# Optimization experiments

Hardware: AMD Instinct MI355X
Metric: run time of the kernel (lower is better)

Reference implementation:

```python
import jax, jax.numpy as jnp
import numpy as np

B, L, D, W = 4, 256, 256, 8  # batch, seq_len, d_model, context_window
NS_EPS = 1e-7


def setup_inputs() -> dict:
    key = jax.random.key(0)
    ks = jax.random.split(key, 12)
    f = lambda k, s: jax.random.normal(k, s, dtype=jnp.float32)
    sD = 1.0 / np.sqrt(D)
    return {
        "x": f(ks[0], (B, L, D)),
        "k_aligned": jnp.tanh(f(ks[1], (B, L, D))),  # QKProjectionLayer applies tanh upstream
        "v": f(ks[2], (B, L, D)),
        "M_prev": f(ks[3], (B, D, D)) * 0.01,
        "S_prev": jnp.zeros((B, D, D), jnp.float32),
        # polynomial feature coeffs: phi(k) = c1*k + c2*k^2 (degree 2, dim-preserving)
        "poly_coeffs": jnp.stack([jnp.ones((D,), jnp.float32), 0.1 * jnp.ones((D,), jnp.float32)])
        + 0.01 * f(ks[4], (2, D)),
        "alpha_W": f(ks[5], (D, D)) * sD, "alpha_b": jnp.zeros((D,), jnp.float32),
        "eta_W": f(ks[6], (D, D)) * sD, "eta_b": jnp.zeros((D,), jnp.float32),
        "theta_W": f(ks[7], (D, D)) * sD, "theta_b": jnp.zeros((D,), jnp.float32),
        "gamma_W": f(ks[8], (D,)) * sD, "gamma_b": jnp.zeros((1,), jnp.float32),
        "out_W": f(ks[9], (D, D)) * sD, "out_b": jnp.zeros((D,), jnp.float32),
    }


def _newton_schulz_1(S):
    # NS_K with K=1: X <- 1.5*X - 0.5*X X^T X after Frobenius normalization
    norm = jnp.sqrt(jnp.sum(S * S, axis=(-2, -1), keepdims=True)) + NS_EPS
    X = S / norm
    return 1.5 * X - 0.5 * jnp.einsum('bij,bkj,bkl->bil', X, X, X)


def reference(x, k_aligned, v, M_prev, S_prev, poly_coeffs,
              alpha_W, alpha_b, eta_W, eta_b, theta_W, theta_b,
              gamma_W, gamma_b, out_W, out_b):
    Bn, Ln, Dn = x.shape
    # polynomial feature layer (dim-preserving, degree 2)
    k_phi = poly_coeffs[0] * k_aligned + poly_coeffs[1] * k_aligned ** 2  # [B,L,D]
    # per-token gates (precomputed, pure linear+sigmoid)
    alpha = jax.nn.sigmoid(x @ alpha_W.T + alpha_b)          # [B,L,D]
    eta = jax.nn.sigmoid(x @ eta_W.T + eta_b) * 0.1          # [B,L,D]
    theta = jax.nn.sigmoid(x @ theta_W.T + theta_b)          # [B,L,D]
    gamma = jax.nn.sigmoid(jnp.einsum('bld,d->bl', x, gamma_W) + gamma_b[0])  # [B,L]
    c_arr = jnp.minimum(jnp.arange(Ln) + 1, W).astype(x.dtype)  # actual window length per step

    to_t = lambda a: jnp.moveaxis(a, 1, 0)  # [B,L,...] -> [L,B,...]
    xs = (to_t(k_phi), to_t(v), to_t(gamma), to_t(alpha), to_t(eta), to_t(theta), c_arr)

    buf_k = jnp.zeros((Bn, W, Dn), x.dtype)  # sliding window of phi(k); zero pads contribute 0
    buf_v = jnp.zeros((Bn, W, Dn), x.dtype)
    buf_g = jnp.zeros((Bn, W), x.dtype)

    def step(carry, xt):
        M, S, bk, bv, bg = carry
        k_t, v_t, g_t, a_t, e_t, th_t, c_t = xt
        bk = jnp.concatenate([bk[:, 1:], k_t[:, None]], axis=1)
        bv = jnp.concatenate([bv[:, 1:], v_t[:, None]], axis=1)
        bg = jnp.concatenate([bg[:, 1:], g_t[:, None]], axis=1)
        # Omega gradient: sum_i gamma_i * (M phi(k_i) - v_i) outer phi(k_i) / c
        pred = jnp.einsum('bde,bwe->bwd', M, bk)
        err = pred - bv
        grad = jnp.einsum('bw,bwd,bwe->bde', bg, err, bk) / c_t
        S = th_t[..., None] * S + grad
        S_ortho = _newton_schulz_1(S)
        M = a_t[..., None] * M - e_t[..., None] * S_ortho
        y = jnp.einsum('bde,be->bd', M, k_t)
        return (M, S, bk, bv, bg), y

    (M, S, _, _, _), ys = jax.lax.scan(step, (M_prev, S_prev, buf_k, buf_v, buf_g), xs)
    output = jnp.moveaxis(ys, 0, 1) @ out_W.T + out_b  # out_proj per token
    return (output, M, S)
```

## Files before the change

### kernel.cpp

```cpp
#include <hip/hip_runtime.h>

#define Bn 4
#define Ln 256
#define Dn 256
#define Wn 8
#define NBLK 64
#define BLD (Bn*Ln*Dn)
#define BDD (Bn*Dn*Dn)

typedef float  floatx4 __attribute__((ext_vector_type(4)));
typedef short  short8  __attribute__((ext_vector_type(8)));

__device__ __forceinline__ float ldc(const float* p) {
    return __hip_atomic_load(p, __ATOMIC_RELAXED, __HIP_MEMORY_SCOPE_AGENT);
}
__device__ __forceinline__ void stc(float* p, float v) {
    __hip_atomic_store(p, v, __ATOMIC_RELAXED, __HIP_MEMORY_SCOPE_AGENT);
}
__device__ __forceinline__ void stc4(float* p, floatx4 v) {
    asm volatile("global_store_dwordx4 %0, %1, off sc0 sc1" :: "v"(p), "v"(v) : "memory");
}
__device__ __forceinline__ void ldc4x4(floatx4& a0, floatx4& a1, floatx4& a2, floatx4& a3,
    const float* p0, const float* p1, const float* p2, const float* p3)
{
    asm volatile(
        "global_load_dwordx4 %0, %4, off sc0 sc1\n\t"
        "global_load_dwordx4 %1, %5, off sc0 sc1\n\t"
        "global_load_dwordx4 %2, %6, off sc0 sc1\n\t"
        "global_load_dwordx4 %3, %7, off sc0 sc1\n\t"
        "s_waitcnt vmcnt(0)"
        : "=&v"(a0), "=&v"(a1), "=&v"(a2), "=&v"(a3)
        : "v"(p0), "v"(p1), "v"(p2), "v"(p3)
        : "memory");
}
__device__ __forceinline__ void ldc4x8(
    floatx4& a0, floatx4& a1, floatx4& a2, floatx4& a3,
    floatx4& b0, floatx4& b1, floatx4& b2, floatx4& b3,
    const float* p0, const float* p1, const float* p2, const float* p3,
    const float* q0, const float* q1, const float* q2, const float* q3)
{
    asm volatile(
        "global_load_dwordx4 %0, %8, off sc0 sc1\n\t"
        "global_load_dwordx4 %1, %9, off sc0 sc1\n\t"
        "global_load_dwordx4 %2, %10, off sc0 sc1\n\t"
        "global_load_dwordx4 %3, %11, off sc0 sc1\n\t"
        "global_load_dwordx4 %4, %12, off sc0 sc1\n\t"
        "global_load_dwordx4 %5, %13, off sc0 sc1\n\t"
        "global_load_dwordx4 %6, %14, off sc0 sc1\n\t"
        "global_load_dwordx4 %7, %15, off sc0 sc1\n\t"
        "s_waitcnt vmcnt(0)"
        : "=&v"(a0), "=&v"(a1), "=&v"(a2), "=&v"(a3),
          "=&v"(b0), "=&v"(b1), "=&v"(b2), "=&v"(b3)
        : "v"(p0), "v"(p1), "v"(p2), "v"(p3),
          "v"(q0), "v"(q1), "v"(q2), "v"(q3)
        : "memory");
}
__device__ __forceinline__ void ldc1x8(
    float& d0, float& d1, float& d2, float& d3,
    float& d4, float& d5, float& d6, float& d7,
    const float* p0, const float* p1, const float* p2, const float* p3,
    const float* p4, const float* p5, const float* p6, const float* p7)
{
    asm volatile(
        "global_load_dword %0, %8, off sc0 sc1\n\t"
        "global_load_dword %1, %9, off sc0 sc1\n\t"
        "global_load_dword %2, %10, off sc0 sc1\n\t"
        "global_load_dword %3, %11, off sc0 sc1\n\t"
        "global_load_dword %4, %12, off sc0 sc1\n\t"
        "global_load_dword %5, %13, off sc0 sc1\n\t"
        "global_load_dword %6, %14, off sc0 sc1\n\t"
        "global_load_dword %7, %15, off sc0 sc1\n\t"
        "s_waitcnt vmcnt(0)"
        : "=&v"(d0), "=&v"(d1), "=&v"(d2), "=&v"(d3),
          "=&v"(d4), "=&v"(d5), "=&v"(d6), "=&v"(d7)
        : "v"(p0), "v"(p1), "v"(p2), "v"(p3),
          "v"(p4), "v"(p5), "v"(p6), "v"(p7)
        : "memory");
}

__device__ __forceinline__ unsigned f2bf(float x) {
    unsigned u = __float_as_uint(x);
    return (u + 0x7FFFu + ((u >> 16) & 1u)) >> 16;
}
__device__ __forceinline__ unsigned long long packbf4(floatx4 v) {
    unsigned lo = f2bf(v[0]) | (f2bf(v[1]) << 16);
    unsigned hi = f2bf(v[2]) | (f2bf(v[3]) << 16);
    return (unsigned long long)lo | ((unsigned long long)hi << 32);
}

__device__ __forceinline__ void grid_sync(unsigned* flags, unsigned k)
{
    asm volatile("s_waitcnt vmcnt(0) lgkmcnt(0)" ::: "memory");
    __syncthreads();
    if (threadIdx.x == 0)
        __hip_atomic_store(&flags[(unsigned)blockIdx.x * 32u], k,
                           __ATOMIC_RELAXED, __HIP_MEMORY_SCOPE_AGENT);
    if (threadIdx.x < NBLK) {
        while (__hip_atomic_load(&flags[(unsigned)threadIdx.x * 32u],
                                 __ATOMIC_RELAXED, __HIP_MEMORY_SCOPE_AGENT) < k)
            __builtin_amdgcn_s_sleep(1);
    }
    __syncthreads();
}

__global__ __launch_bounds__(256) void kphi_gamma_kernel(
    const float* __restrict__ k_al, const float* __restrict__ x,
    const float* __restrict__ poly, const float* __restrict__ gW,
    const float* __restrict__ gb, float* __restrict__ kphi,
    float* __restrict__ gamma)
{
    int wg = blockIdx.x, tid = threadIdx.x;
    int wave = tid >> 6, lane = tid & 63;
    int n = wg * 4 + wave;
    float gacc = 0.f;
#pragma unroll
    for (int c = 0; c < 4; ++c) {
        int e = lane + 64 * c;
        float kv = k_al[n * Dn + e];
        kphi[n * Dn + e] = poly[e] * kv + poly[Dn + e] * kv * kv;
        gacc += x[n * Dn + e] * gW[e];
    }
#pragma unroll
    for (int off = 32; off; off >>= 1) gacc += __shfl_xor(gacc, off);
    if (lane == 0) gamma[n] = 1.f / (1.f + expf(-(gacc + gb[0])));
}

template <int ACT>
__global__ __launch_bounds__(256) void gemm_act_kernel(
    const float* __restrict__ In, const float* __restrict__ Wm,
    const float* __restrict__ bias, float* __restrict__ Out)
{
    __shared__ float ldsX[32 * 64];
    __shared__ float ldsW[64 * 65];
    int n0 = blockIdx.x * 32;
    int m0 = blockIdx.y * 64;
    int tid = threadIdx.x;
    float acc[8] = {0, 0, 0, 0, 0, 0, 0, 0};
    for (int j0 = 0; j0 < 256; j0 += 64) {
#pragma unroll
        for (int q = 0; q < 2; ++q) {
            int fi = tid + 256 * q; int row = fi >> 4; int c4 = (fi & 15) << 2;
            *(float4*)&ldsX[row * 64 + c4] =
                *(const float4*)&In[(n0 + row) * 256 + j0 + c4];
        }
#pragma unroll
        for (int q = 0; q < 4; ++q) {
            int fi = tid + 256 * q; int row = fi >> 4; int c4 = (fi & 15) << 2;
            float4 vv = *(const float4*)&Wm[(m0 + row) * 256 + j0 + c4];
            ldsW[(c4 + 0) * 65 + row] = vv.x;
            ldsW[(c4 + 1) * 65 + row] = vv.y;
            ldsW[(c4 + 2) * 65 + row] = vv.z;
            ldsW[(c4 + 3) * 65 + row] = vv.w;
        }
        __syncthreads();
        int m = tid & 63, ng = tid >> 6;
        for (int j = 0; j < 64; ++j) {
            float wv = ldsW[j * 65 + m];
#pragma unroll
            for (int r = 0; r < 8; ++r) acc[r] += ldsX[(ng * 8 + r) * 64 + j] * wv;
        }
        __syncthreads();
    }
    int m = tid & 63, ng = tid >> 6;
    float bv = bias[m0 + m];
#pragma unroll
    for (int r = 0; r < 8; ++r) {
        float vv = acc[r] + bv;
        if (ACT == 1) vv = 1.f / (1.f + expf(-vv));
        if (ACT == 2) vv = 0.1f / (1.f + expf(-vv));
        Out[(n0 + ng * 8 + r) * 256 + m0 + m] = vv;
    }
}

__global__ __launch_bounds__(256) void prologue_kernel(
    const float* __restrict__ Mprev, const float* __restrict__ Sprev,
    float* __restrict__ M, float* __restrict__ S, float* __restrict__ ST,
    float* __restrict__ ys, float* __restrict__ normbuf,
    unsigned* __restrict__ flags)
{
    int gidx = blockIdx.x * 256 + threadIdx.x;
    ((float4*)M)[gidx] = ((const float4*)Mprev)[gidx];
    ((float4*)S)[gidx] = ((const float4*)Sprev)[gidx];
    float4 z = {0.f, 0.f, 0.f, 0.f};
    ((float4*)ys)[gidx] = z;
    {
        int o = gidx * 4;
        int bb = o >> 16, rm = o & 65535, l = rm >> 8, k = rm & 255;
        float4 stv;
        stv.x = Sprev[bb * 65536 + (k + 0) * 256 + l];
        stv.y = Sprev[bb * 65536 + (k + 1) * 256 + l];
        stv.z = Sprev[bb * 65536 + (k + 2) * 256 + l];
        stv.w = Sprev[bb * 65536 + (k + 3) * 256 + l];
        ((float4*)ST)[gidx] = stv;
    }
    if (gidx < Ln * Bn) normbuf[gidx] = 0.f;
    if (gidx < NBLK * 32) flags[gidx] = 0u;
}

__global__ void __launch_bounds__(256, 1) scan_kernel(
    const float* __restrict__ kphi, const float* __restrict__ vin,
    const float* __restrict__ gammaB, const float* __restrict__ alphaB,
    const float* __restrict__ etaB, const float* __restrict__ thetaB,
    float* __restrict__ Mg, float* __restrict__ Sg, float* __restrict__ STg,
    float* __restrict__ T0g, float* __restrict__ T1g,
    float* __restrict__ u_buf, float* __restrict__ a_buf,
    float* __restrict__ K_buf, float* __restrict__ normbuf,
    float* __restrict__ ysg, unsigned* __restrict__ flags)
{
    __shared__ float smem[11072];
    const int wg = blockIdx.x, tid = threadIdx.x;
    const int b = wg >> 4;
    const int rem = wg & 15;
    const int i0 = (rem >> 2) * 64, l0 = (rem & 3) * 64;
    const int d0 = rem << 4;
    const int wid = tid >> 6, lane = tid & 63;
    const int rb = (tid >> 4) << 2;
    const int kb = (tid & 15) << 2;
    char* TtB  = (char*)(smem + 6464);
    char* StlB = (char*)(smem + 8768);
    unsigned kbar = 0;

    {
        floatx4 acc[4];
#pragma unroll
        for (int lt = 0; lt < 4; ++lt) acc[lt] = (floatx4){0.f, 0.f, 0.f, 0.f};
        const float* Sb = Sg + (size_t)b * Dn * Dn;
        for (int kc = 0; kc < 256; kc += 64) {
            floatx4 t0, t1, t2, t3, s0, s1, s2, s3;
            ldc4x8(t0, t1, t2, t3, s0, s1, s2, s3,
                   &Sb[(i0 + rb + 0) * Dn + kc + kb], &Sb[(i0 + rb + 1) * Dn + kc + kb],
                   &Sb[(i0 + rb + 2) * Dn + kc + kb], &Sb[(i0 + rb + 3) * Dn + kc + kb],
                   &Sb[(l0 + rb + 0) * Dn + kc + kb], &Sb[(l0 + rb + 1) * Dn + kc + kb],
                   &Sb[(l0 + rb + 2) * Dn + kc + kb], &Sb[(l0 + rb + 3) * Dn + kc + kb]);
            *(unsigned long long*)(TtB + (rb + 0) * 144 + kb * 2) = packbf4(t0);
            *(unsigned long long*)(TtB + (rb + 1) * 144 + kb * 2) = packbf4(t1);
            *(unsigned long long*)(TtB + (rb + 2) * 144 + kb * 2) = packbf4(t2);
            *(unsigned long long*)(TtB + (rb + 3) * 144 + kb * 2) = packbf4(t3);
            *(unsigned long long*)(StlB + (rb + 0) * 144 + kb * 2) = packbf4(s0);
            *(unsigned long long*)(StlB + (rb + 1) * 144 + kb * 2) = packbf4(s1);
            *(unsigned long long*)(StlB + (rb + 2) * 144 + kb * 2) = packbf4(s2);
            *(unsigned long long*)(StlB + (rb + 3) * 144 + kb * 2) = packbf4(s3);
            __syncthreads();
            const int arow = wid * 16 + (lane & 15);
#pragma unroll
            for (int ks = 0; ks < 2; ++ks) {
                const int kloc = ks * 32 + ((lane >> 4) << 3);
                short8 af = *(const short8*)(TtB + arow * 144 + kloc * 2);
#pragma unroll
                for (int lt = 0; lt < 4; ++lt) {
                    short8 bf = *(const short8*)(StlB + (lt * 16 + (lane & 15)) * 144 + kloc * 2);
                    acc[lt] = __builtin_amdgcn_mfma_f32_16x16x32_bf16(af, bf, acc[lt], 0, 0, 0);
                }
            }
            __syncthreads();
        }
        const int ibr = i0 + wid * 16 + ((lane >> 4) << 2);
        const int lc = lane & 15;
#pragma unroll
        for (int lt = 0; lt < 4; ++lt)
#pragma unroll
            for (int g = 0; g < 4; ++g)
                stc(&T0g[((size_t)b * Dn + ibr + g) * Dn + l0 + lt * 16 + lc], acc[lt][g]);
    }
    grid_sync(flags, ++kbar);

    for (int t = 0; t < Ln; ++t) {
        const int cwin = (t + 1 < Wn) ? (t + 1) : Wn;
        const float invc = 1.f / (float)cwin;

        {
            float* kW  = smem;
            float* Mst = smem + 2080;
            float* Sst = smem + 6240;
            float* us  = smem + 10400;
            float* as_ = smem + 10528;
            float* ths = smem + 10656;
#pragma unroll
            for (int q = 0; q < 2; ++q) {
                int w = q * 4 + (tid >> 6);
                int c4 = (tid & 63) << 2;
                int tk = t - 7 + w;
                floatx4 kv = {0.f, 0.f, 0.f, 0.f};
                if (tk >= 0) kv = *(const floatx4*)&kphi[(b * Ln + tk) * Dn + c4];
                *(floatx4*)&kW[w * 260 + c4] = kv;
            }
            if (tid < 16) ths[tid] = thetaB[(b * Ln + t) * Dn + d0 + tid];
            {
                const float* mb = &Mg[((size_t)b * Dn + d0) * Dn];
                const float* sb = &Sg[((size_t)b * Dn + d0) * Dn];
                int ra = tid >> 6, c4 = (tid & 63) << 2;
                floatx4 m0, m1, m2, m3, s0, s1, s2, s3;
                ldc4x8(m0, m1, m2, m3, s0, s1, s2, s3,
                       &mb[(ra + 0) * Dn + c4], &mb[(ra + 4) * Dn + c4],
                       &mb[(ra + 8) * Dn + c4], &mb[(ra + 12) * Dn + c4],
                       &sb[(ra + 0) * Dn + c4], &sb[(ra + 4) * Dn + c4],
                       &sb[(ra + 8) * Dn + c4], &sb[(ra + 12) * Dn + c4]);
                *(floatx4*)&Mst[(ra + 0) * 260 + c4] = m0;
                *(floatx4*)&Mst[(ra + 4) * 260 + c4] = m1;
                *(floatx4*)&Mst[(ra + 8) * 260 + c4] = m2;
                *(floatx4*)&Mst[(ra + 12) * 260 + c4] = m3;
                *(floatx4*)&Sst[(ra + 0) * 260 + c4] = s0;
                *(floatx4*)&Sst[(ra + 4) * 260 + c4] = s1;
                *(floatx4*)&Sst[(ra + 8) * 260 + c4] = s2;
                *(floatx4*)&Sst[(ra + 12) * 260 + c4] = s3;
            }
            __syncthreads();
            {
                const int w = tid >> 5, r = (tid >> 1) & 15, eh = tid & 1;
                const int eb = eh * 128;
                float em = 0.f, eq = 0.f;
                for (int j = 0; j < 128; j += 4) {
                    floatx4 kv = *(const floatx4*)&kW[w * 260 + eb + j];
                    floatx4 mv = *(const floatx4*)&Mst[r * 260 + eb + j];
                    floatx4 sv = *(const floatx4*)&Sst[r * 260 + eb + j];
                    em += kv[0] * mv[0] + kv[1] * mv[1] + kv[2] * mv[2] + kv[3] * mv[3];
                    eq += kv[0] * sv[0] + kv[1] * sv[1] + kv[2] * sv[2] + kv[3] * sv[3];
                }
                em += __shfl_xor(em, 1);
                eq += __shfl_xor(eq, 1);
                if (eh == 0) {
                    int tok = t - 7 + w;
                    float uu = 0.f;
                    if (tok >= 0) {
                        float ev = em - vin[(b * Ln + tok) * Dn + d0 + r];
                        uu = gammaB[b * Ln + tok] * invc * ev;
                    }
                    float aa = ths[r] * eq;
                    us[w * 16 + r] = uu;
                    as_[w * 16 + r] = aa;
                    stc(&u_buf[(b * 8 + w) * Dn + d0 + r], uu);
                    stc(&a_buf[(b * 8 + w) * Dn + d0 + r], aa);
                }
            }
            if (rem == 0 && tid < 64) {
                int wa = tid >> 3, wb2 = tid & 7;
                float g = 0.f;
                for (int j = 0; j < 256; j += 4) {
                    floatx4 x1 = *(const floatx4*)&kW[wa * 260 + j];
                    floatx4 x2 = *(const floatx4*)&kW[wb2 * 260 + j];
                    g += x1[0] * x2[0] + x1[1] * x2[1] + x1[2] * x2[2] + x1[3] * x2[3];
                }
                stc(&K_buf[b * 64 + tid], g);
            }
            __syncthreads();
            float* Snew = Mst;
            {
                int r = tid >> 4, m = tid & 15;
                float th = ths[r];
                float uu[8];
#pragma unroll
                for (int w = 0; w < 8; ++w) uu[w] = us[w * 16 + r];
                float sumsq = 0.f;
                for (int c = 0; c < 16; ++c) {
                    int e = m + 16 * c;
                    float sv = th * Sst[r * 260 + e];
#pragma unroll
                    for (int w = 0; w < 8; ++w) sv += uu[w] * kW[w * 260 + e];
                    Snew[r * 260 + e] = sv;
                    sumsq += sv * sv;
                }
#pragma unroll
                for (int off = 32; off; off >>= 1) sumsq += __shfl_xor(sumsq, off);
                if ((tid & 63) == 0) atomicAdd(&normbuf[t * Bn + b], sumsq);
            }
            __syncthreads();
            {
                int r = tid >> 4, ec = (tid & 15) * 16;
                float* Sp = &Sg[((size_t)b * Dn + d0 + r) * Dn + ec];
#pragma unroll
                for (int c = 0; c < 4; ++c)
                    stc4(&Sp[c * 4], *(floatx4*)&Snew[r * 260 + ec + c * 4]);
            }
            {
                int lq = tid >> 4, r = tid & 15;
#pragma unroll
                for (int j = 0; j < 16; ++j) {
                    int l = lq * 16 + j;
                    stc(&STg[((size_t)b * Dn + l) * Dn + d0 + r], Snew[r * 260 + l]);
                }
            }
        }
        grid_sync(flags, ++kbar);

        {
            float* uv  = smem;
            float* av  = smem + 2048;
            float* cv  = smem + 4096;
            float* thv = smem + 6144;
            float* Kl  = smem + 6400;
            const float* Told = ((t & 1) ? T1g : T0g) + (size_t)b * Dn * Dn;
            float*       Tnew = ((t & 1) ? T0g : T1g) + (size_t)b * Dn * Dn;
            const float* STb = STg + (size_t)b * Dn * Dn;
            float nrmsq = ldc(&normbuf[t * Bn + b]);
            {
                int fi0 = tid, fi1 = 256 + tid, fi2 = tid, fi3 = 256 + tid;
                floatx4 v0, v1, v2, v3;
                ldc4x4(v0, v1, v2, v3,
                       &u_buf[b * 2048 + fi0 * 4], &u_buf[b * 2048 + fi1 * 4],
                       &a_buf[b * 2048 + fi2 * 4], &a_buf[b * 2048 + fi3 * 4]);
                *(floatx4*)&uv[fi0 * 4] = v0;
                *(floatx4*)&uv[fi1 * 4] = v1;
                *(floatx4*)&av[fi2 * 4] = v2;
                *(floatx4*)&av[fi3 * 4] = v3;
                if (tid < 64) {
                    *(floatx4*)&thv[tid * 4] = *(const floatx4*)&thetaB[(b * Ln + t) * Dn + tid * 4];
                    Kl[tid] = ldc(&K_buf[b * 64 + tid]);
                }
            }
            __syncthreads();
#pragma unroll
            for (int q = 0; q < 8; ++q) {
                int idx = q * 256 + tid;
                int w = idx >> 8, e = idx & 255;
                float s = av[idx];
#pragma unroll
                for (int w2 = 0; w2 < 8; ++w2) s += 0.5f * Kl[w * 8 + w2] * uv[w2 * 256 + e];
                cv[idx] = s;
            }
            __syncthreads();
            floatx4 acc[4];
#pragma unroll
            for (int lt = 0; lt < 4; ++lt) acc[lt] = (floatx4){0.f, 0.f, 0.f, 0.f};
            for (int kc = 0; kc < 256; kc += 64) {
                floatx4 tv0, tv1, tv2, tv3, s0, s1, s2, s3;
                ldc4x8(tv0, tv1, tv2, tv3, s0, s1, s2, s3,
                       &Told[(i0 + rb + 0) * Dn + kc + kb], &Told[(i0 + rb + 1) * Dn + kc + kb],
                       &Told[(i0 + rb + 2) * Dn + kc + kb], &Told[(i0 + rb + 3) * Dn + kc + kb],
                       &STb[(l0 + rb + 0) * Dn + kc + kb], &STb[(l0 + rb + 1) * Dn + kc + kb],
                       &STb[(l0 + rb + 2) * Dn + kc + kb], &STb[(l0 + rb + 3) * Dn + kc + kb]);
                floatx4 tvv[4] = {tv0, tv1, tv2, tv3};
                floatx4 thk = *(floatx4*)&thv[kc + kb];
#pragma unroll
                for (int x = 0; x < 4; ++x) {
                    float thi = thv[i0 + rb + x];
                    tvv[x] = (thi * thk) * tvv[x];
                }
#pragma unroll
                for (int w = 0; w < 8; ++w) {
                    floatx4 ui = *(floatx4*)&uv[w * 256 + i0 + rb];
                    floatx4 ci = *(floatx4*)&cv[w * 256 + i0 + rb];
                    floatx4 uk = *(floatx4*)&uv[w * 256 + kc + kb];
                    floatx4 ck = *(floatx4*)&cv[w * 256 + kc + kb];
#pragma unroll
                    for (int x = 0; x < 4; ++x)
                        tvv[x] += ui[x] * ck + ci[x] * uk;
                }
                if (l0 == 0) {
#pragma unroll
                    for (int x = 0; x < 4; ++x)
                        stc4(&Tnew[(i0 + rb + x) * Dn + kc + kb], tvv[x]);
                }
                floatx4 svv_[4] = {s0, s1, s2, s3};
#pragma unroll
                for (int x = 0; x < 4; ++x) {
                    *(unsigned long long*)(TtB + (rb + x) * 144 + kb * 2) = packbf4(tvv[x]);
                    *(unsigned long long*)(StlB + (rb + x) * 144 + kb * 2) = packbf4(svv_[x]);
                }
                __syncthreads();
                const int arow = wid * 16 + (lane & 15);
#pragma unroll
                for (int ks = 0; ks < 2; ++ks) {
                    const int kloc = ks * 32 + ((lane >> 4) << 3);
                    short8 af = *(const short8*)(TtB + arow * 144 + kloc * 2);
#pragma unroll
                    for (int lt = 0; lt < 4; ++lt) {
                        short8 bf = *(const short8*)(StlB + (lt * 16 + (lane & 15)) * 144 + kloc * 2);
                        acc[lt] = __builtin_amdgcn_mfma_f32_16x16x32_bf16(af, bf, acc[lt], 0, 0, 0);
                    }
                }
                __syncthreads();
            }
            {
                float nrm = sqrtf(nrmsq) + 1e-7f;
                float inv_n = 1.f / nrm;
                float w1 = 1.5f * inv_n;
                float w3 = 0.5f * inv_n * inv_n * inv_n;
                const int ibr = i0 + wid * 16 + ((lane >> 4) << 2);
                const int lc = lane & 15;
                float* Mb = Mg + (size_t)b * Dn * Dn;
                const float* sp[16]; float* mp[16];
#pragma unroll
                for (int lt = 0; lt < 4; ++lt)
#pragma unroll
                    for (int g = 0; g < 4; ++g) {
                        int l = l0 + lt * 16 + lc;
                        sp[lt * 4 + g] = &STb[l * Dn + ibr + g];
                        mp[lt * 4 + g] = &Mb[(ibr + g) * Dn + l];
                    }
                float svv[16], mvv[16];
                ldc1x8(svv[0], svv[1], svv[2], svv[3], svv[4], svv[5], svv[6], svv[7],
                       sp[0], sp[1], sp[2], sp[3], sp[4], sp[5], sp[6], sp[7]);
                ldc1x8(svv[8], svv[9], svv[10], svv[11], svv[12], svv[13], svv[14], svv[15],
                       sp[8], sp[9], sp[10], sp[11], sp[12], sp[13], sp[14], sp[15]);
                ldc1x8(mvv[0], mvv[1], mvv[2], mvv[3], mvv[4], mvv[5], mvv[6], mvv[7],
                       mp[0], mp[1], mp[2], mp[3], mp[4], mp[5], mp[6], mp[7]);
                ldc1x8(mvv[8], mvv[9], mvv[10], mvv[11], mvv[12], mvv[13], mvv[14], mvv[15],
                       mp[8], mp[9], mp[10], mp[11], mp[12], mp[13], mp[14], mp[15]);
                float alv[4], etv[4];
#pragma unroll
                for (int g = 0; g < 4; ++g) {
                    alv[g] = alphaB[(b * Ln + t) * Dn + ibr + g];
                    etv[g] = etaB[(b * Ln + t) * Dn + ibr + g];
                }
                float kvr[4];
#pragma unroll
                for (int lt = 0; lt < 4; ++lt)
                    kvr[lt] = kphi[(b * Ln + t) * Dn + l0 + lt * 16 + lc];
                float py[4] = {0.f, 0.f, 0.f, 0.f};
#pragma unroll
                for (int lt = 0; lt < 4; ++lt)
#pragma unroll
                    for (int g = 0; g < 4; ++g) {
                        int idx = lt * 4 + g;
                        float ns = w1 * svv[idx] - w3 * acc[lt][g];
                        float mn = alv[g] * mvv[idx] - etv[g] * ns;
                        stc(mp[idx], mn);
                        py[g] += mn * kvr[lt];
                    }
#pragma unroll
                for (int g = 0; g < 4; ++g) {
                    float p = py[g];
                    p += __shfl_xor(p, 1); p += __shfl_xor(p, 2);
                    p += __shfl_xor(p, 4); p += __shfl_xor(p, 8);
                    if (lc == 0) atomicAdd(&ysg[(b * Ln + t) * Dn + ibr + g], p);
                }
            }
        }
        grid_sync(flags, ++kbar);
    }
}

extern "C" void kernel_launch(void* const* d_in, const int* in_sizes, int n_in,
                              void* d_out, int out_size, void* d_ws, size_t ws_size,
                              hipStream_t stream)
{
    const float* x       = (const float*)d_in[0];
    const float* k_al    = (const float*)d_in[1];
    const float* v       = (const float*)d_in[2];
    const float* M_prev  = (const float*)d_in[3];
    const float* S_prev  = (const float*)d_in[4];
    const float* poly    = (const float*)d_in[5];
    const float* alpha_W = (const float*)d_in[6];
    const float* alpha_b = (const float*)d_in[7];
    const float* eta_W   = (const float*)d_in[8];
    const float* eta_b   = (const float*)d_in[9];
    const float* theta_W = (const float*)d_in[10];
    const float* theta_b = (const float*)d_in[11];
    const float* gamma_W = (const float*)d_in[12];
    const float* gamma_b = (const float*)d_in[13];
    const float* out_W   = (const float*)d_in[14];
    const float* out_b   = (const float*)d_in[15];

    float* ws = (float*)d_ws;
    float* kphi    = ws;
    float* alphaB  = kphi   + BLD;
    float* etaB    = alphaB + BLD;
    float* thetaB  = etaB   + BLD;
    float* gammaB  = thetaB + BLD;
    float* STws    = gammaB + Bn * Ln;
    float* T0ws    = STws   + BDD;
    float* T1ws    = T0ws   + BDD;
    float* ysws    = T1ws   + BDD;
    float* u_bufp  = ysws   + BLD;
    float* a_bufp  = u_bufp + Bn*Wn*Dn;
    float* K_bufp  = a_bufp + Bn*Wn*Dn;
    float* normbuf = K_bufp + Bn*64;
    unsigned* flags = (unsigned*)(normbuf + Ln * Bn);

    float* out_y = (float*)d_out;
    float* Mout  = out_y + BLD;
    float* Sout  = Mout + BDD;

    hipLaunchKernelGGL(kphi_gamma_kernel, dim3(256), dim3(256), 0, stream,
                       k_al, x, poly, gamma_W, gamma_b, kphi, gammaB);
    hipLaunchKernelGGL((gemm_act_kernel<1>), dim3(32, 4), dim3(256), 0, stream,
                       x, alpha_W, alpha_b, alphaB);
    hipLaunchKernelGGL((gemm_act_kernel<2>), dim3(32, 4), dim3(256), 0, stream,
                       x, eta_W, eta_b, etaB);
    hipLaunchKernelGGL((gemm_act_kernel<1>), dim3(32, 4), dim3(256), 0, stream,
                       x, theta_W, theta_b, thetaB);
    hipLaunchKernelGGL(prologue_kernel, dim3(256), dim3(256), 0, stream,
                       M_prev, S_prev, Mout, Sout, STws, ysws, normbuf, flags);

    hipLaunchKernelGGL(scan_kernel, dim3(NBLK), dim3(256), 0, stream,
                       kphi, v, gammaB, alphaB, etaB, thetaB,
                       Mout, Sout, STws, T0ws, T1ws,
                       u_bufp, a_bufp, K_bufp, normbuf, ysws, flags);

    hipLaunchKernelGGL((gemm_act_kernel<0>), dim3(32, 4), dim3(256), 0, stream,
                       ysws, out_W, out_b, out_y);
}
```

Measured before the change: 5.978 ms.

## Keep M and S tiles register-resident across scan steps, precompute window Gram matrix

The persistent scan kernel now holds each block's slice of M and S in registers for all steps, where before it reloaded and stored them through global memory every step. It also keeps the Newton-Schulz Gram product T in LDS and stages S in bf16. The window Gram matrix of phi(k) moves to a separate pre-kernel, and the M·phi(k) error terms for the next step are computed early and double-buffered through atomics. The aim is to remove per-step global round-trips and cut the critical path between grid barriers, at the cost of more register and LDS pressure and more complex cross-step atomics.

Measured after the change: 6.245 ms. 1.04x slower.

```diff
diff --git a/kernel.cpp b/kernel.cpp
--- a/kernel.cpp
+++ b/kernel.cpp
@@ -55,28 +55,6 @@
           "v"(q0), "v"(q1), "v"(q2), "v"(q3)
         : "memory");
 }
-__device__ __forceinline__ void ldc1x8(
-    float& d0, float& d1, float& d2, float& d3,
-    float& d4, float& d5, float& d6, float& d7,
-    const float* p0, const float* p1, const float* p2, const float* p3,
-    const float* p4, const float* p5, const float* p6, const float* p7)
-{
-    asm volatile(
-        "global_load_dword %0, %8, off sc0 sc1\n\t"
-        "global_load_dword %1, %9, off sc0 sc1\n\t"
-        "global_load_dword %2, %10, off sc0 sc1\n\t"
-        "global_load_dword %3, %11, off sc0 sc1\n\t"
-        "global_load_dword %4, %12, off sc0 sc1\n\t"
-        "global_load_dword %5, %13, off sc0 sc1\n\t"
-        "global_load_dword %6, %14, off sc0 sc1\n\t"
-        "global_load_dword %7, %15, off sc0 sc1\n\t"
-        "s_waitcnt vmcnt(0)"
-        : "=&v"(d0), "=&v"(d1), "=&v"(d2), "=&v"(d3),
-          "=&v"(d4), "=&v"(d5), "=&v"(d6), "=&v"(d7)
-        : "v"(p0), "v"(p1), "v"(p2), "v"(p3),
-          "v"(p4), "v"(p5), "v"(p6), "v"(p7)
-        : "memory");
-}
 
 __device__ __forceinline__ unsigned f2bf(float x) {
     unsigned u = __float_as_uint(x);
@@ -87,6 +65,7 @@
     unsigned hi = f2bf(v[2]) | (f2bf(v[3]) << 16);
     return (unsigned long long)lo | ((unsigned long long)hi << 32);
 }
+union BF8 { short8 s8; unsigned long long u[2]; };
 
 __device__ __forceinline__ void grid_sync(unsigned* flags, unsigned k)
 {
@@ -172,95 +151,155 @@
     }
 }
 
+__global__ __launch_bounds__(64) void kgram_kernel(
+    const float* __restrict__ kphi, float* __restrict__ Kall)
+{
+    int t = blockIdx.x, b = blockIdx.y, tid = threadIdx.x;
+    int wa = tid >> 3, wb = tid & 7;
+    int ta = t - 7 + wa, tb = t - 7 + wb;
+    float g = 0.f;
+    if (ta >= 0 && tb >= 0) {
+        const float* pa = &kphi[(b * Ln + ta) * Dn];
+        const float* pb = &kphi[(b * Ln + tb) * Dn];
+        for (int j = 0; j < Dn; j += 4) {
+            floatx4 x1 = *(const floatx4*)&pa[j];
+            floatx4 x2 = *(const floatx4*)&pb[j];
+            g += x1[0]*x2[0] + x1[1]*x2[1] + x1[2]*x2[2] + x1[3]*x2[3];
+        }
+    }
+    Kall[(b * Ln + t) * 64 + tid] = g;
+}
+
 __global__ __launch_bounds__(256) void prologue_kernel(
-    const float* __restrict__ Mprev, const float* __restrict__ Sprev,
-    float* __restrict__ M, float* __restrict__ S, float* __restrict__ ST,
-    float* __restrict__ ys, float* __restrict__ normbuf,
-    unsigned* __restrict__ flags)
+    float* __restrict__ ys, float* __restrict__ errp,
+    float* __restrict__ normbuf, unsigned* __restrict__ flags)
 {
     int gidx = blockIdx.x * 256 + threadIdx.x;
-    ((float4*)M)[gidx] = ((const float4*)Mprev)[gidx];
-    ((float4*)S)[gidx] = ((const float4*)Sprev)[gidx];
     float4 z = {0.f, 0.f, 0.f, 0.f};
     ((float4*)ys)[gidx] = z;
-    {
-        int o = gidx * 4;
-        int bb = o >> 16, rm = o & 65535, l = rm >> 8, k = rm & 255;
-        float4 stv;
-        stv.x = Sprev[bb * 65536 + (k + 0) * 256 + l];
-        stv.y = Sprev[bb * 65536 + (k + 1) * 256 + l];
-        stv.z = Sprev[bb * 65536 + (k + 2) * 256 + l];
-        stv.w = Sprev[bb * 65536 + (k + 3) * 256 + l];
-        ((float4*)ST)[gidx] = stv;
-    }
-    if (gidx < Ln * Bn) normbuf[gidx] = 0.f;
-    if (gidx < NBLK * 32) flags[gidx] = 0u;
-}
+    if (gidx < 4096) ((float4*)errp)[gidx] = z;
+    if (gidx < 256)  ((float4*)normbuf)[gidx] = z;
+    if (gidx < 512)  {
+        uint4 zu = {0u,0u,0u,0u};
+        ((uint4*)flags)[gidx] = zu;
+    }
+}
+
+#define OFF_T      0
+#define OFF_ST     16640
+#define OFF_UV     25088
+#define OFF_AV     27136
+#define OFF_CV     29184
+#define OFF_TH     31232
+#define OFF_KT     31488
+#define OFF_KW2    31744
+#define OFF_KWA    33792
+#define OFF_KL     35872
+#define OFF_SRED   35936
 
 __global__ void __launch_bounds__(256, 1) scan_kernel(
     const float* __restrict__ kphi, const float* __restrict__ vin,
     const float* __restrict__ gammaB, const float* __restrict__ alphaB,
     const float* __restrict__ etaB, const float* __restrict__ thetaB,
-    float* __restrict__ Mg, float* __restrict__ Sg, float* __restrict__ STg,
-    float* __restrict__ T0g, float* __restrict__ T1g,
+    const float* __restrict__ Kall,
+    const float* __restrict__ Mprev, const float* __restrict__ Sprev,
+    unsigned short* __restrict__ STg,
     float* __restrict__ u_buf, float* __restrict__ a_buf,
-    float* __restrict__ K_buf, float* __restrict__ normbuf,
-    float* __restrict__ ysg, unsigned* __restrict__ flags)
-{
-    __shared__ float smem[11072];
+    float* __restrict__ errp_g, float* __restrict__ normbuf,
+    float* __restrict__ ysg, unsigned* __restrict__ flags,
+    float* __restrict__ outM, float* __restrict__ outS)
+{
+    __shared__ float smem[36000];
+    float* T_lds = smem + OFF_T;
+    float* uv    = smem + OFF_UV;
+    float* av    = smem + OFF_AV;
+    float* cv    = smem + OFF_CV;
+    float* thv   = smem + OFF_TH;
+    float* kT    = smem + OFF_KT;
+    float* kW2   = smem + OFF_KW2;
+    float* kWA   = smem + OFF_KWA;
+    float* Kl    = smem + OFF_KL;
+    float* sred  = smem + OFF_SRED;
+
     const int wg = blockIdx.x, tid = threadIdx.x;
-    const int b = wg >> 4;
+    const int b   = wg >> 4;
     const int rem = wg & 15;
     const int i0 = (rem >> 2) * 64, l0 = (rem & 3) * 64;
     const int d0 = rem << 4;
     const int wid = tid >> 6, lane = tid & 63;
-    const int rb = (tid >> 4) << 2;
-    const int kb = (tid & 15) << 2;
-    char* TtB  = (char*)(smem + 6464);
-    char* StlB = (char*)(smem + 8768);
+    const int lme = lane & 15, hi = lane >> 4;
+    const int ibr = i0 + wid * 16 + (hi << 2);
+    const int r  = tid >> 4, m = tid & 15;
+    const int e0 = m * 16;
     unsigned kbar = 0;
 
+    floatx4 S_reg[4];
+    float   M_reg[16];
+
     {
-        floatx4 acc[4];
-#pragma unroll
-        for (int lt = 0; lt < 4; ++lt) acc[lt] = (floatx4){0.f, 0.f, 0.f, 0.f};
-        const float* Sb = Sg + (size_t)b * Dn * Dn;
-        for (int kc = 0; kc < 256; kc += 64) {
-            floatx4 t0, t1, t2, t3, s0, s1, s2, s3;
-            ldc4x8(t0, t1, t2, t3, s0, s1, s2, s3,
-                   &Sb[(i0 + rb + 0) * Dn + kc + kb], &Sb[(i0 + rb + 1) * Dn + kc + kb],
-                   &Sb[(i0 + rb + 2) * Dn + kc + kb], &Sb[(i0 + rb + 3) * Dn + kc + kb],
-                   &Sb[(l0 + rb + 0) * Dn + kc + kb], &Sb[(l0 + rb + 1) * Dn + kc + kb],
-                   &Sb[(l0 + rb + 2) * Dn + kc + kb], &Sb[(l0 + rb + 3) * Dn + kc + kb]);
-            *(unsigned long long*)(TtB + (rb + 0) * 144 + kb * 2) = packbf4(t0);
-            *(unsigned long long*)(TtB + (rb + 1) * 144 + kb * 2) = packbf4(t1);
-            *(unsigned long long*)(TtB + (rb + 2) * 144 + kb * 2) = packbf4(t2);
-            *(unsigned long long*)(TtB + (rb + 3) * 144 + kb * 2) = packbf4(t3);
-            *(unsigned long long*)(StlB + (rb + 0) * 144 + kb * 2) = packbf4(s0);
-            *(unsigned long long*)(StlB + (rb + 1) * 144 + kb * 2) = packbf4(s1);
-            *(unsigned long long*)(StlB + (rb + 2) * 144 + kb * 2) = packbf4(s2);
-            *(unsigned long long*)(StlB + (rb + 3) * 144 + kb * 2) = packbf4(s3);
-            __syncthreads();
-            const int arow = wid * 16 + (lane & 15);
-#pragma unroll
-            for (int ks = 0; ks < 2; ++ks) {
-                const int kloc = ks * 32 + ((lane >> 4) << 3);
-                short8 af = *(const short8*)(TtB + arow * 144 + kloc * 2);
+#pragma unroll
+        for (int cq = 0; cq < 4; ++cq)
+            S_reg[cq] = *(const floatx4*)&Sprev[(size_t)(b*256 + d0 + r)*256 + e0 + cq*4];
+#pragma unroll
+        for (int lt = 0; lt < 4; ++lt)
+#pragma unroll
+            for (int g = 0; g < 4; ++g)
+                M_reg[lt*4+g] = Mprev[(size_t)(b*256 + ibr + g)*256 + l0 + lt*16 + lme];
+
+        for (int g4 = 0; g4 < 4; ++g4) {
+            floatx4 acc[4];
+#pragma unroll
+            for (int lt = 0; lt < 4; ++lt) acc[lt] = (floatx4){0.f,0.f,0.f,0.f};
+#pragma unroll
+            for (int kc = 0; kc < 8; ++kc) {
+                int kb2 = kc*32 + hi*8;
+                floatx4 a0 = *(const floatx4*)&Sprev[(size_t)(b*256 + i0 + wid*16 + lme)*256 + kb2];
+                floatx4 a1 = *(const floatx4*)&Sprev[(size_t)(b*256 + i0 + wid*16 + lme)*256 + kb2 + 4];
+                BF8 ua; ua.u[0] = packbf4(a0); ua.u[1] = packbf4(a1);
 #pragma unroll
                 for (int lt = 0; lt < 4; ++lt) {
-                    short8 bf = *(const short8*)(StlB + (lt * 16 + (lane & 15)) * 144 + kloc * 2);
-                    acc[lt] = __builtin_amdgcn_mfma_f32_16x16x32_bf16(af, bf, acc[lt], 0, 0, 0);
-                }
-            }
-            __syncthreads();
-        }
-        const int ibr = i0 + wid * 16 + ((lane >> 4) << 2);
-        const int lc = lane & 15;
-#pragma unroll
-        for (int lt = 0; lt < 4; ++lt)
-#pragma unroll
-            for (int g = 0; g < 4; ++g)
-                stc(&T0g[((size_t)b * Dn + ibr + g) * Dn + l0 + lt * 16 + lc], acc[lt][g]);
+                    int brow = g4*64 + lt*16 + lme;
+                    floatx4 b0 = *(const floatx4*)&Sprev[(size_t)(b*256 + brow)*256 + kb2];
+                    floatx4 b1 = *(const floatx4*)&Sprev[(size_t)(b*256 + brow)*256 + kb2 + 4];
+                    BF8 ub; ub.u[0] = packbf4(b0); ub.u[1] = packbf4(b1);
+                    acc[lt] = __builtin_amdgcn_mfma_f32_16x16x32_bf16(ua.s8, ub.s8, acc[lt], 0,0,0);
+                }
+            }
+#pragma unroll
+            for (int lt = 0; lt < 4; ++lt)
+#pragma unroll
+                for (int g = 0; g < 4; ++g)
+                    T_lds[(wid*16 + (hi<<2) + g)*260 + g4*64 + lt*16 + lme] = acc[lt][g];
+        }
+
+#pragma unroll
+        for (int q = 0; q < 2; ++q) {
+            int w = q*4 + (tid >> 6);
+            int c4 = (tid & 63) << 2;
+            floatx4 kv = {0.f,0.f,0.f,0.f};
+            if (w == 7) kv = *(const floatx4*)&kphi[(size_t)(b*Ln)*Dn + c4];
+            *(floatx4*)&kW2[w*256 + c4] = kv;
+        }
+        __syncthreads();
+#pragma unroll
+        for (int w = 0; w < 8; ++w) {
+            float pd[4] = {0.f,0.f,0.f,0.f};
+#pragma unroll
+            for (int lt = 0; lt < 4; ++lt) {
+                float kv2 = kW2[w*256 + l0 + lt*16 + lme];
+#pragma unroll
+                for (int g = 0; g < 4; ++g) pd[g] += M_reg[lt*4+g] * kv2;
+            }
+#pragma unroll
+            for (int g = 0; g < 4; ++g) {
+                pd[g] += __shfl_xor(pd[g], 1); pd[g] += __shfl_xor(pd[g], 2);
+                pd[g] += __shfl_xor(pd[g], 4); pd[g] += __shfl_xor(pd[g], 8);
+            }
+            if (lme == 0)
+#pragma unroll
+                for (int g = 0; g < 4; ++g)
+                    atomicAdd(&errp_g[(size_t)(0*4 + b)*2048 + w*256 + ibr + g], pd[g]);
+        }
     }
     grid_sync(flags, ++kbar);
 
@@ -269,260 +308,271 @@
         const float invc = 1.f / (float)cwin;
 
         {
-            float* kW  = smem;
-            float* Mst = smem + 2080;
-            float* Sst = smem + 6240;
-            float* us  = smem + 10400;
-            float* as_ = smem + 10528;
-            float* ths = smem + 10656;
 #pragma unroll
             for (int q = 0; q < 2; ++q) {
-                int w = q * 4 + (tid >> 6);
+                int w = q*4 + (tid >> 6);
                 int c4 = (tid & 63) << 2;
                 int tk = t - 7 + w;
-                floatx4 kv = {0.f, 0.f, 0.f, 0.f};
-                if (tk >= 0) kv = *(const floatx4*)&kphi[(b * Ln + tk) * Dn + c4];
-                *(floatx4*)&kW[w * 260 + c4] = kv;
-            }
-            if (tid < 16) ths[tid] = thetaB[(b * Ln + t) * Dn + d0 + tid];
+                floatx4 kv = {0.f,0.f,0.f,0.f};
+                if (tk >= 0) kv = *(const floatx4*)&kphi[(size_t)(b*Ln + tk)*Dn + c4];
+                *(floatx4*)&kWA[w*260 + c4] = kv;
+            }
+            __syncthreads();
+
             {
-                const float* mb = &Mg[((size_t)b * Dn + d0) * Dn];
-                const float* sb = &Sg[((size_t)b * Dn + d0) * Dn];
-                int ra = tid >> 6, c4 = (tid & 63) << 2;
-                floatx4 m0, m1, m2, m3, s0, s1, s2, s3;
-                ldc4x8(m0, m1, m2, m3, s0, s1, s2, s3,
-                       &mb[(ra + 0) * Dn + c4], &mb[(ra + 4) * Dn + c4],
-                       &mb[(ra + 8) * Dn + c4], &mb[(ra + 12) * Dn + c4],
-                       &sb[(ra + 0) * Dn + c4], &sb[(ra + 4) * Dn + c4],
-                       &sb[(ra + 8) * Dn + c4], &sb[(ra + 12) * Dn + c4]);
-                *(floatx4*)&Mst[(ra + 0) * 260 + c4] = m0;
-                *(floatx4*)&Mst[(ra + 4) * 260 + c4] = m1;
-                *(floatx4*)&Mst[(ra + 8) * 260 + c4] = m2;
-                *(floatx4*)&Mst[(ra + 12) * 260 + c4] = m3;
-                *(floatx4*)&Sst[(ra + 0) * 260 + c4] = s0;
-                *(floatx4*)&Sst[(ra + 4) * 260 + c4] = s1;
-                *(floatx4*)&Sst[(ra + 8) * 260 + c4] = s2;
-                *(floatx4*)&Sst[(ra + 12) * 260 + c4] = s3;
+                float qw[8] = {0,0,0,0,0,0,0,0};
+#pragma unroll
+                for (int cq = 0; cq < 4; ++cq) {
+                    floatx4 sv = S_reg[cq];
+#pragma unroll
+                    for (int w = 0; w < 8; ++w) {
+                        floatx4 kv = *(const floatx4*)&kWA[w*260 + e0 + cq*4];
+                        qw[w] += sv[0]*kv[0] + sv[1]*kv[1] + sv[2]*kv[2] + sv[3]*kv[3];
+                    }
+                }
+#pragma unroll
+                for (int w = 0; w < 8; ++w) {
+                    qw[w] += __shfl_xor(qw[w], 1); qw[w] += __shfl_xor(qw[w], 2);
+                    qw[w] += __shfl_xor(qw[w], 4); qw[w] += __shfl_xor(qw[w], 8);
+                }
+                if (m < 8) {
+                    float th = thetaB[(size_t)(b*Ln + t)*Dn + d0 + r];
+                    stc(&a_buf[(size_t)(b*8 + m)*256 + d0 + r], th * qw[m]);
+                }
+            }
+            if (tid < 128) {
+                int w = tid >> 4, rr = tid & 15;
+                float* epp = &errp_g[(size_t)((t&1)*4 + b)*2048 + w*256 + d0 + rr];
+                float ep = ldc(epp);
+                stc(epp, 0.f);
+                int tok = t - 7 + w;
+                float uu = 0.f;
+                if (tok >= 0)
+                    uu = gammaB[b*Ln + tok] * invc *
+                         (ep - vin[(size_t)(b*Ln + tok)*Dn + d0 + rr]);
+                uv[w*16 + rr] = uu;
+                stc(&u_buf[(size_t)(b*8 + w)*256 + d0 + rr], uu);
             }
             __syncthreads();
+
             {
-                const int w = tid >> 5, r = (tid >> 1) & 15, eh = tid & 1;
-                const int eb = eh * 128;
-                float em = 0.f, eq = 0.f;
-                for (int j = 0; j < 128; j += 4) {
-                    floatx4 kv = *(const floatx4*)&kW[w * 260 + eb + j];
-                    floatx4 mv = *(const floatx4*)&Mst[r * 260 + eb + j];
-                    floatx4 sv = *(const floatx4*)&Sst[r * 260 + eb + j];
-                    em += kv[0] * mv[0] + kv[1] * mv[1] + kv[2] * mv[2] + kv[3] * mv[3];
-                    eq += kv[0] * sv[0] + kv[1] * sv[1] + kv[2] * sv[2] + kv[3] * sv[3];
-                }
-                em += __shfl_xor(em, 1);
-                eq += __shfl_xor(eq, 1);
-                if (eh == 0) {
-                    int tok = t - 7 + w;
-                    float uu = 0.f;
-                    if (tok >= 0) {
-                        float ev = em - vin[(b * Ln + tok) * Dn + d0 + r];
-                        uu = gammaB[b * Ln + tok] * invc * ev;
-                    }
-                    float aa = ths[r] * eq;
-                    us[w * 16 + r] = uu;
-                    as_[w * 16 + r] = aa;
-                    stc(&u_buf[(b * 8 + w) * Dn + d0 + r], uu);
-                    stc(&a_buf[(b * 8 + w) * Dn + d0 + r], aa);
-                }
-            }
-            if (rem == 0 && tid < 64) {
-                int wa = tid >> 3, wb2 = tid & 7;
-                float g = 0.f;
-                for (int j = 0; j < 256; j += 4) {
-                    floatx4 x1 = *(const floatx4*)&kW[wa * 260 + j];
-                    floatx4 x2 = *(const floatx4*)&kW[wb2 * 260 + j];
-                    g += x1[0] * x2[0] + x1[1] * x2[1] + x1[2] * x2[2] + x1[3] * x2[3];
-                }
-                stc(&K_buf[b * 64 + tid], g);
+                float th = thetaB[(size_t)(b*Ln + t)*Dn + d0 + r];
+                float uu[8];
+#pragma unroll
+                for (int w = 0; w < 8; ++w) uu[w] = uv[w*16 + r];
+                float sumsq = 0.f;
+#pragma unroll
+                for (int cq = 0; cq < 4; ++cq) {
+                    floatx4 sv = th * S_reg[cq];
+#pragma unroll
+                    for (int w = 0; w < 8; ++w) {
+                        floatx4 kv = *(const floatx4*)&kWA[w*260 + e0 + cq*4];
+                        sv += uu[w] * kv;
+                    }
+                    S_reg[cq] = sv;
+                    sumsq += sv[0]*sv[0] + sv[1]*sv[1] + sv[2]*sv[2] + sv[3]*sv[3];
+                }
+#pragma unroll
+                for (int off = 32; off; off >>= 1) sumsq += __shfl_xor(sumsq, off);
+                if ((tid & 63) == 0) atomicAdd(&normbuf[t*4 + b], sumsq);
+            }
+
+            {
+                float* Sl = smem + OFF_ST;
+#pragma unroll
+                for (int cq = 0; cq < 4; ++cq)
+                    *(floatx4*)&Sl[r*260 + e0 + cq*4] = S_reg[cq];
+                __syncthreads();
+                int l = tid;
+                unsigned dw[8];
+#pragma unroll
+                for (int j = 0; j < 8; ++j)
+                    dw[j] = f2bf(Sl[(2*j)*260 + l]) | (f2bf(Sl[(2*j+1)*260 + l]) << 16);
+                floatx4 p0 = { __uint_as_float(dw[0]), __uint_as_float(dw[1]),
+                               __uint_as_float(dw[2]), __uint_as_float(dw[3]) };
+                floatx4 p1 = { __uint_as_float(dw[4]), __uint_as_float(dw[5]),
+                               __uint_as_float(dw[6]), __uint_as_float(dw[7]) };
+                char* dstp = (char*)STg + ((size_t)(b*256 + l)*256 + d0)*2;
+                stc4((float*)dstp, p0);
+                stc4((float*)(dstp + 16), p1);
+            }
+            if (t == Ln - 1) {
+#pragma unroll
+                for (int cq = 0; cq < 4; ++cq)
+                    *(floatx4*)&outS[(size_t)(b*256 + d0 + r)*256 + e0 + cq*4] = S_reg[cq];
+            }
+        }
+        grid_sync(flags, ++kbar);
+
+        {
+            {
+                int lq = tid >> 2, kq = (tid & 3) * 64;
+                const char* src = (const char*)STg + ((size_t)(b*256 + l0 + lq)*256 + kq)*2;
+                floatx4 r0,r1,r2,r3,r4,r5,r6,r7;
+                ldc4x8(r0,r1,r2,r3,r4,r5,r6,r7,
+                       (const float*)(src+0),  (const float*)(src+16),
+                       (const float*)(src+32), (const float*)(src+48),
+                       (const float*)(src+64), (const float*)(src+80),
+                       (const float*)(src+96), (const float*)(src+112));
+                char* dst = (char*)(smem + OFF_ST) + (lq*264 + kq)*2;
+                *(floatx4*)(dst+0)  = r0; *(floatx4*)(dst+16) = r1;
+                *(floatx4*)(dst+32) = r2; *(floatx4*)(dst+48) = r3;
+                *(floatx4*)(dst+64) = r4; *(floatx4*)(dst+80) = r5;
+                *(floatx4*)(dst+96) = r6; *(floatx4*)(dst+112)= r7;
+
+                floatx4 u0,u1,a0,a1;
+                ldc4x4(u0,u1,a0,a1,
+                       &u_buf[(size_t)b*2048 + tid*8], &u_buf[(size_t)b*2048 + tid*8 + 4],
+                       &a_buf[(size_t)b*2048 + tid*8], &a_buf[(size_t)b*2048 + tid*8 + 4]);
+                *(floatx4*)&uv[tid*8]     = u0; *(floatx4*)&uv[tid*8 + 4] = u1;
+                *(floatx4*)&av[tid*8]     = a0; *(floatx4*)&av[tid*8 + 4] = a1;
+
+                if (tid < 64) {
+                    *(floatx4*)&thv[tid*4] = *(const floatx4*)&thetaB[(size_t)(b*Ln + t)*Dn + tid*4];
+                    *(floatx4*)&kT[tid*4]  = *(const floatx4*)&kphi[(size_t)(b*Ln + t)*Dn + tid*4];
+                }
+                if (tid < 16)
+                    *(floatx4*)&Kl[tid*4] = *(const floatx4*)&Kall[(size_t)(b*Ln + t)*64 + tid*4];
+                if (t < Ln - 1) {
+#pragma unroll
+                    for (int q = 0; q < 2; ++q) {
+                        int w = q*4 + (tid >> 6);
+                        int c4 = (tid & 63) << 2;
+                        int tk = t + 1 - 7 + w;
+                        floatx4 kv = {0.f,0.f,0.f,0.f};
+                        if (tk >= 0) kv = *(const floatx4*)&kphi[(size_t)(b*Ln + tk)*Dn + c4];
+                        *(floatx4*)&kW2[w*256 + c4] = kv;
+                    }
+                }
+                if (tid == 0) sred[0] = ldc(&normbuf[t*4 + b]);
             }
             __syncthreads();
-            float* Snew = Mst;
-            {
-                int r = tid >> 4, m = tid & 15;
-                float th = ths[r];
-                float uu[8];
-#pragma unroll
-                for (int w = 0; w < 8; ++w) uu[w] = us[w * 16 + r];
-                float sumsq = 0.f;
-                for (int c = 0; c < 16; ++c) {
-                    int e = m + 16 * c;
-                    float sv = th * Sst[r * 260 + e];
-#pragma unroll
-                    for (int w = 0; w < 8; ++w) sv += uu[w] * kW[w * 260 + e];
-                    Snew[r * 260 + e] = sv;
-                    sumsq += sv * sv;
-                }
-#pragma unroll
-                for (int off = 32; off; off >>= 1) sumsq += __shfl_xor(sumsq, off);
-                if ((tid & 63) == 0) atomicAdd(&normbuf[t * Bn + b], sumsq);
-            }
-            __syncthreads();
-            {
-                int r = tid >> 4, ec = (tid & 15) * 16;
-                float* Sp = &Sg[((size_t)b * Dn + d0 + r) * Dn + ec];
-#pragma unroll
-                for (int c = 0; c < 4; ++c)
-                    stc4(&Sp[c * 4], *(floatx4*)&Snew[r * 260 + ec + c * 4]);
-            }
-            {
-                int lq = tid >> 4, r = tid & 15;
-#pragma unroll
-                for (int j = 0; j < 16; ++j) {
-                    int l = lq * 16 + j;
-                    stc(&STg[((size_t)b * Dn + l) * Dn + d0 + r], Snew[r * 260 + l]);
-                }
-            }
-        }
-        grid_sync(flags, ++kbar);
-
-        {
-            float* uv  = smem;
-            float* av  = smem + 2048;
-            float* cv  = smem + 4096;
-            float* thv = smem + 6144;
-            float* Kl  = smem + 6400;
-            const float* Told = ((t & 1) ? T1g : T0g) + (size_t)b * Dn * Dn;
-            float*       Tnew = ((t & 1) ? T0g : T1g) + (size_t)b * Dn * Dn;
-            const float* STb = STg + (size_t)b * Dn * Dn;
-            float nrmsq = ldc(&normbuf[t * Bn + b]);
-            {
-                int fi0 = tid, fi1 = 256 + tid, fi2 = tid, fi3 = 256 + tid;
-                floatx4 v0, v1, v2, v3;
-                ldc4x4(v0, v1, v2, v3,
-                       &u_buf[b * 2048 + fi0 * 4], &u_buf[b * 2048 + fi1 * 4],
-                       &a_buf[b * 2048 + fi2 * 4], &a_buf[b * 2048 + fi3 * 4]);
-                *(floatx4*)&uv[fi0 * 4] = v0;
-                *(floatx4*)&uv[fi1 * 4] = v1;
-                *(floatx4*)&av[fi2 * 4] = v2;
-                *(floatx4*)&av[fi3 * 4] = v3;
-                if (tid < 64) {
-                    *(floatx4*)&thv[tid * 4] = *(const floatx4*)&thetaB[(b * Ln + t) * Dn + tid * 4];
-                    Kl[tid] = ldc(&K_buf[b * 64 + tid]);
-                }
-            }
-            __syncthreads();
+
 #pragma unroll
             for (int q = 0; q < 8; ++q) {
-                int idx = q * 256 + tid;
+                int idx = q*256 + tid;
                 int w = idx >> 8, e = idx & 255;
                 float s = av[idx];
 #pragma unroll
-                for (int w2 = 0; w2 < 8; ++w2) s += 0.5f * Kl[w * 8 + w2] * uv[w2 * 256 + e];
+                for (int w2 = 0; w2 < 8; ++w2)
+                    s += 0.5f * Kl[w*8 + w2] * uv[w2*256 + e];
                 cv[idx] = s;
             }
             __syncthreads();
+
+            {
+                int ig = tid >> 4;
+                int iloc0 = ig * 4;
+                int kg = (tid & 15) * 16;
+                floatx4 thi = *(const floatx4*)&thv[i0 + iloc0];
+                floatx4 thk[4], Trow[4][4];
+#pragma unroll
+                for (int j = 0; j < 4; ++j) thk[j] = *(const floatx4*)&thv[kg + 4*j];
+#pragma unroll
+                for (int ii = 0; ii < 4; ++ii)
+#pragma unroll
+                    for (int j = 0; j < 4; ++j) {
+                        Trow[ii][j] = *(const floatx4*)&T_lds[(iloc0+ii)*260 + kg + 4*j];
+                        Trow[ii][j] = (thi[ii] * thk[j]) * Trow[ii][j];
+                    }
+#pragma unroll
+                for (int w = 0; w < 8; ++w) {
+                    floatx4 ui4 = *(const floatx4*)&uv[w*256 + i0 + iloc0];
+                    floatx4 ci4 = *(const floatx4*)&cv[w*256 + i0 + iloc0];
+                    floatx4 uk[4], ck[4];
+#pragma unroll
+                    for (int j = 0; j < 4; ++j) {
+                        uk[j] = *(const floatx4*)&uv[w*256 + kg + 4*j];
+                        ck[j] = *(const floatx4*)&cv[w*256 + kg + 4*j];
+                    }
+#pragma unroll
+                    for (int ii = 0; ii < 4; ++ii)
+#pragma unroll
+                        for (int j = 0; j < 4; ++j)
+                            Trow[ii][j] += ui4[ii]*ck[j] + ci4[ii]*uk[j];
+                }
+#pragma unroll
+                for (int ii = 0; ii < 4; ++ii)
+#pragma unroll
+                    for (int j = 0; j < 4; ++j)
+                        *(floatx4*)&T_lds[(iloc0+ii)*260 + kg + 4*j] = Trow[ii][j];
+            }
+            __syncthreads();
+
             floatx4 acc[4];
 #pragma unroll
-            for (int lt = 0; lt < 4; ++lt) acc[lt] = (floatx4){0.f, 0.f, 0.f, 0.f};
-            for (int kc = 0; kc < 256; kc += 64) {
-                floatx4 tv0, tv1, tv2, tv3, s0, s1, s2, s3;
-                ldc4x8(tv0, tv1, tv2, tv3, s0, s1, s2, s3,
-                       &Told[(i0 + rb + 0) * Dn + kc + kb], &Told[(i0 + rb + 1) * Dn + kc + kb],
-                       &Told[(i0 + rb + 2) * Dn + kc + kb], &Told[(i0 + rb + 3) * Dn + kc + kb],
-                       &STb[(l0 + rb + 0) * Dn + kc + kb], &STb[(l0 + rb + 1) * Dn + kc + kb],
-                       &STb[(l0 + rb + 2) * Dn + kc + kb], &STb[(l0 + rb + 3) * Dn + kc + kb]);
-                floatx4 tvv[4] = {tv0, tv1, tv2, tv3};
-                floatx4 thk = *(floatx4*)&thv[kc + kb];
-#pragma unroll
-                for (int x = 0; x < 4; ++x) {
-                    float thi = thv[i0 + rb + x];
-                    tvv[x] = (thi * thk) * tvv[x];
-                }
-#pragma unroll
-                for (int w = 0; w < 8; ++w) {
-                    floatx4 ui = *(floatx4*)&uv[w * 256 + i0 + rb];
-                    floatx4 ci = *(floatx4*)&cv[w * 256 + i0 + rb];
-                    floatx4 uk = *(floatx4*)&uv[w * 256 + kc + kb];
-                    floatx4 ck = *(floatx4*)&cv[w * 256 + kc + kb];
-#pragma unroll
-                    for (int x = 0; x < 4; ++x)
-                        tvv[x] += ui[x] * ck + ci[x] * uk;
-                }
-                if (l0 == 0) {
-#pragma unroll
-                    for (int x = 0; x < 4; ++x)
-                        stc4(&Tnew[(i0 + rb + x) * Dn + kc + kb], tvv[x]);
-                }
-                floatx4 svv_[4] = {s0, s1, s2, s3};
-#pragma unroll
-                for (int x = 0; x < 4; ++x) {
-                    *(unsigned long long*)(TtB + (rb + x) * 144 + kb * 2) = packbf4(tvv[x]);
-                    *(unsigned long long*)(StlB + (rb + x) * 144 + kb * 2) = packbf4(svv_[x]);
-                }
-                __syncthreads();
-                const int arow = wid * 16 + (lane & 15);
-#pragma unroll
-                for (int ks = 0; ks < 2; ++ks) {
-                    const int kloc = ks * 32 + ((lane >> 4) << 3);
-                    short8 af = *(const short8*)(TtB + arow * 144 + kloc * 2);
-#pragma unroll
-                    for (int lt = 0; lt < 4; ++lt) {
-                        short8 bf = *(const short8*)(StlB + (lt * 16 + (lane & 15)) * 144 + kloc * 2);
-                        acc[lt] = __builtin_amdgcn_mfma_f32_16x16x32_bf16(af, bf, acc[lt], 0, 0, 0);
-                    }
-                }
-                __syncthreads();
-            }
+            for (int lt = 0; lt < 4; ++lt) acc[lt] = (floatx4){0.f,0.f,0.f,0.f};
+#pragma unroll
+            for (int kc = 0; kc < 8; ++kc) {
+                int kb2 = kc*32 + hi*8;
+                floatx4 a0 = *(const floatx4*)&T_lds[(wid*16 + lme)*260 + kb2];
+                floatx4 a1 = *(const floatx4*)&T_lds[(wid*16 + lme)*260 + kb2 + 4];
+                BF8 ua; ua.u[0] = packbf4(a0); ua.u[1] = packbf4(a1);
+#pragma unroll
+                for (int lt = 0; lt < 4; ++lt) {
+                    short8 bf = *(const short8*)((const char*)(smem + OFF_ST)
+                                  + ((lt*16 + lme)*264 + kb2)*2);
+                    acc[lt] = __builtin_amdgcn_mfma_f32_16x16x32_bf16(ua.s8, bf, acc[lt], 0,0,0);
+                }
+            }
+
             {
-                float nrm = sqrtf(nrmsq) + 1e-7f;
+                float nsq = sred[0];
+                float nrm = sqrtf(nsq) + 1e-7f;
                 float inv_n = 1.f / nrm;
                 float w1 = 1.5f * inv_n;
                 float w3 = 0.5f * inv_n * inv_n * inv_n;
-                const int ibr = i0 + wid * 16 + ((lane >> 4) << 2);
-                const int lc = lane & 15;
-                float* Mb = Mg + (size_t)b * Dn * Dn;
-                const float* sp[16]; float* mp[16];
+                float alv[4], etv[4], kvr[4];
+#pragma unroll
+                for (int g = 0; g < 4; ++g) {
+                    alv[g] = alphaB[(size_t)(b*Ln + t)*Dn + ibr + g];
+                    etv[g] = etaB[(size_t)(b*Ln + t)*Dn + ibr + g];
+                }
+#pragma unroll
+                for (int lt = 0; lt < 4; ++lt) kvr[lt] = kT[l0 + lt*16 + lme];
+                float py[4] = {0.f,0.f,0.f,0.f};
 #pragma unroll
                 for (int lt = 0; lt < 4; ++lt)
 #pragma unroll
                     for (int g = 0; g < 4; ++g) {
-                        int l = l0 + lt * 16 + lc;
-                        sp[lt * 4 + g] = &STb[l * Dn + ibr + g];
-                        mp[lt * 4 + g] = &Mb[(ibr + g) * Dn + l];
-                    }
-                float svv[16], mvv[16];
-                ldc1x8(svv[0], svv[1], svv[2], svv[3], svv[4], svv[5], svv[6], svv[7],
-                       sp[0], sp[1], sp[2], sp[3], sp[4], sp[5], sp[6], sp[7]);
-                ldc1x8(svv[8], svv[9], svv[10], svv[11], svv[12], svv[13], svv[14], svv[15],
-                       sp[8], sp[9], sp[10], sp[11], sp[12], sp[13], sp[14], sp[15]);
-                ldc1x8(mvv[0], mvv[1], mvv[2], mvv[3], mvv[4], mvv[5], mvv[6], mvv[7],
-                       mp[0], mp[1], mp[2], mp[3], mp[4], mp[5], mp[6], mp[7]);
-                ldc1x8(mvv[8], mvv[9], mvv[10], mvv[11], mvv[12], mvv[13], mvv[14], mvv[15],
-                       mp[8], mp[9], mp[10], mp[11], mp[12], mp[13], mp[14], mp[15]);
-                float alv[4], etv[4];
+                        int l_loc = lt*16 + lme;
+                        unsigned short sb = *(const unsigned short*)
+                            ((const char*)(smem + OFF_ST) + (l_loc*264 + ibr + g)*2);
+                        float s_il = __uint_as_float(((unsigned)sb) << 16);
+                        float ns = w1 * s_il - w3 * acc[lt][g];
+                        float mn = alv[g] * M_reg[lt*4+g] - etv[g] * ns;
+                        M_reg[lt*4+g] = mn;
+                        py[g] += mn * kvr[lt];
+                        if (t == Ln - 1)
+                            outM[(size_t)(b*256 + ibr + g)*256 + l0 + l_loc] = mn;
+                    }
 #pragma unroll
                 for (int g = 0; g < 4; ++g) {
-                    alv[g] = alphaB[(b * Ln + t) * Dn + ibr + g];
-                    etv[g] = etaB[(b * Ln + t) * Dn + ibr + g];
-                }
-                float kvr[4];
-#pragma unroll
-                for (int lt = 0; lt < 4; ++lt)
-                    kvr[lt] = kphi[(b * Ln + t) * Dn + l0 + lt * 16 + lc];
-                float py[4] = {0.f, 0.f, 0.f, 0.f};
-#pragma unroll
-                for (int lt = 0; lt < 4; ++lt)
+                    py[g] += __shfl_xor(py[g], 1); py[g] += __shfl_xor(py[g], 2);
+                    py[g] += __shfl_xor(py[g], 4); py[g] += __shfl_xor(py[g], 8);
+                    if (lme == 0) atomicAdd(&ysg[(size_t)(b*Ln + t)*Dn + ibr + g], py[g]);
+                }
+            }
+
+            if (t < Ln - 1) {
+#pragma unroll
+                for (int w = 0; w < 8; ++w) {
+                    float pd[4] = {0.f,0.f,0.f,0.f};
+#pragma unroll
+                    for (int lt = 0; lt < 4; ++lt) {
+                        float kv2 = kW2[w*256 + l0 + lt*16 + lme];
+#pragma unroll
+                        for (int g = 0; g < 4; ++g) pd[g] += M_reg[lt*4+g] * kv2;
+                    }
 #pragma unroll
                     for (int g = 0; g < 4; ++g) {
-                        int idx = lt * 4 + g;
-                        float ns = w1 * svv[idx] - w3 * acc[lt][g];
-                        float mn = alv[g] * mvv[idx] - etv[g] * ns;
-                        stc(mp[idx], mn);
-                        py[g] += mn * kvr[lt];
-                    }
-#pragma unroll
-                for (int g = 0; g < 4; ++g) {
-                    float p = py[g];
-                    p += __shfl_xor(p, 1); p += __shfl_xor(p, 2);
-                    p += __shfl_xor(p, 4); p += __shfl_xor(p, 8);
-                    if (lc == 0) atomicAdd(&ysg[(b * Ln + t) * Dn + ibr + g], p);
+                        pd[g] += __shfl_xor(pd[g], 1); pd[g] += __shfl_xor(pd[g], 2);
+                        pd[g] += __shfl_xor(pd[g], 4); pd[g] += __shfl_xor(pd[g], 8);
+                    }
+                    if (lme == 0)
+#pragma unroll
+                        for (int g = 0; g < 4; ++g)
+                            atomicAdd(&errp_g[(size_t)(((t+1)&1)*4 + b)*2048 + w*256 + ibr + g], pd[g]);
                 }
             }
         }
@@ -557,19 +607,18 @@
     float* etaB    = alphaB + BLD;
     float* thetaB  = etaB   + BLD;
     float* gammaB  = thetaB + BLD;
-    float* STws    = gammaB + Bn * Ln;
-    float* T0ws    = STws   + BDD;
-    float* T1ws    = T0ws   + BDD;
-    float* ysws    = T1ws   + BDD;
-    float* u_bufp  = ysws   + BLD;
+    float* Kall    = gammaB + Bn*Ln;
+    float* STg_f   = Kall   + Bn*Ln*64;
+    float* u_bufp  = STg_f  + 131072;
     float* a_bufp  = u_bufp + Bn*Wn*Dn;
-    float* K_bufp  = a_bufp + Bn*Wn*Dn;
-    float* normbuf = K_bufp + Bn*64;
-    unsigned* flags = (unsigned*)(normbuf + Ln * Bn);
+    float* errp    = a_bufp + Bn*Wn*Dn;
+    float* normbuf = errp   + 16384;
+    float* ysws    = normbuf + Ln*Bn;
+    unsigned* flags = (unsigned*)(ysws + BLD);
 
     float* out_y = (float*)d_out;
-    float* Mout  = out_y + BLD;
-    float* Sout  = Mout + BDD;
+    float* outM  = out_y + BLD;
+    float* outS  = outM + BDD;
 
     hipLaunchKernelGGL(kphi_gamma_kernel, dim3(256), dim3(256), 0, stream,
                        k_al, x, poly, gamma_W, gamma_b, kphi, gammaB);
@@ -579,13 +628,16 @@
                        x, eta_W, eta_b, etaB);
     hipLaunchKernelGGL((gemm_act_kernel<1>), dim3(32, 4), dim3(256), 0, stream,
                        x, theta_W, theta_b, thetaB);
+    hipLaunchKernelGGL(kgram_kernel, dim3(Ln, Bn), dim3(64), 0, stream,
+                       kphi, Kall);
     hipLaunchKernelGGL(prologue_kernel, dim3(256), dim3(256), 0, stream,
-                       M_prev, S_prev, Mout, Sout, STws, ysws, normbuf, flags);
+                       ysws, errp, normbuf, flags);
 
     hipLaunchKernelGGL(scan_kernel, dim3(NBLK), dim3(256), 0, stream,
-                       kphi, v, gammaB, alphaB, etaB, thetaB,
-                       Mout, Sout, STws, T0ws, T1ws,
-                       u_bufp, a_bufp, K_bufp, normbuf, ysws, flags);
+                       kphi, v, gammaB, alphaB, etaB, thetaB, Kall,
+                       M_prev, S_prev, (unsigned short*)STg_f,
+                       u_bufp, a_bufp, errp, normbuf, ysws, flags,
+                       outM, outS);
 
     hipLaunchKernelGGL((gemm_act_kernel<0>), dim3(32, 4), dim3(256), 0, stream,
                        ysws, out_W, out_b, out_y);
```
